# Performance work log

Measured on AMD Instinct MI355X. Metric: run time of the kernel, lower is better.

## Reference

```python
import jax, jax.numpy as jnp
import numpy as np

N = 100000   # nodes
E = 1600000  # edges (avg in-degree 16)
IN, H, C = 128, 128, 40
K = 2        # TAGConv hops (DGL default)


def setup_inputs() -> dict:
    key = jax.random.key(0)
    ks = jax.random.split(key, 7)
    in_feat = jax.random.normal(ks[0], (N, IN), dtype=jnp.float32)
    src = jax.random.randint(ks[1], (E,), 0, N)
    dst = jax.random.randint(ks[2], (E,), 0, N)
    # TAGConv linear: concat of (K+1) hop features -> out
    W1 = jax.random.normal(ks[3], ((K + 1) * IN, H), dtype=jnp.float32) / np.float32(np.sqrt((K + 1) * IN))
    b1 = jnp.zeros((H,), dtype=jnp.float32)
    W2 = jax.random.normal(ks[4], ((K + 1) * H, C), dtype=jnp.float32) / np.float32(np.sqrt((K + 1) * H))
    b2 = jnp.zeros((C,), dtype=jnp.float32)
    return {"in_feat": in_feat, "src": src, "dst": dst,
            "W1": W1, "b1": b1, "W2": W2, "b2": b2}


def _tagconv(x, src, dst, norm, W, b):
    feats = [x]
    h = x
    for _ in range(K):
        h = norm[:, None] * h                               # [N, d]
        h = jax.ops.segment_sum(h[src], dst, num_segments=N)  # SpMM via gather+scatter
        h = norm[:, None] * h
        feats.append(h)
    return jnp.concatenate(feats, axis=-1) @ W + b


def reference(in_feat, src, dst, W1, b1, W2, b2):
    deg = jax.ops.segment_sum(jnp.ones((E,), jnp.float32), dst, num_segments=N)
    norm = jnp.where(deg > 0, deg ** -0.5, 0.0)             # D^{-1/2}, inf -> 0
    h = jax.nn.relu(_tagconv(in_feat, src, dst, norm, W1, b1))
    h = jax.nn.relu(_tagconv(h, src, dst, norm, W2, b2))
    return jnp.mean(h, axis=0, keepdims=True)               # dgl.mean_nodes -> [1, C]
```

## Files before the change

kernel.cpp:

```cpp
#include <hip/hip_runtime.h>

typedef unsigned short u16;
typedef __attribute__((ext_vector_type(8))) short bf16x8;
typedef __attribute__((ext_vector_type(4))) float f32x4;

#define CSR_CHUNK 12288

__device__ inline u16 f2bf(float f) {
    union { float f; unsigned u; } v; v.f = f;
    unsigned r = v.u + 0x7fff + ((v.u >> 16) & 1);
    return (u16)(r >> 16);
}
__device__ inline float bflo(unsigned u) {
    union { unsigned u; float f; } v; v.u = u << 16; return v.f;
}
__device__ inline float bfhi(unsigned u) {
    union { unsigned u; float f; } v; v.u = u & 0xffff0000u; return v.f;
}
__device__ inline float bfs(u16 x) { return bflo((unsigned)x); }

__global__ void zero_int_k(int* __restrict__ p, int n) {
    int i = blockIdx.x * 256 + threadIdx.x;
    if (i < n) p[i] = 0;
}

__global__ __launch_bounds__(256) void bucket_cnt_k(
    const int* __restrict__ dst, int* __restrict__ bcnt, int E, int nbuck) {
    __shared__ int hist[1024];
    int e0 = blockIdx.x * CSR_CHUNK;
    int e1 = min(e0 + CSR_CHUNK, E);
    for (int i = threadIdx.x; i < nbuck; i += 256) hist[i] = 0;
    __syncthreads();
    for (int e = e0 + threadIdx.x; e < e1; e += 256)
        atomicAdd(&hist[dst[e] >> 7], 1);
    __syncthreads();
    for (int i = threadIdx.x; i < nbuck; i += 256) {
        int c = hist[i];
        if (c) atomicAdd(&bcnt[i], c);
    }
}

__global__ void bscan_k(const int* __restrict__ bcnt, int* __restrict__ bptr,
                        int* __restrict__ bcur, int nb, int E) {
    __shared__ int lds[256];
    int t = threadIdx.x;
    int base = t * 4;
    int v[4];
    int s = 0;
#pragma unroll
    for (int i = 0; i < 4; ++i) {
        v[i] = s;
        int idx = base + i;
        s += (idx < nb) ? bcnt[idx] : 0;
    }
    int x = s;
    lds[t] = x;
    __syncthreads();
    for (int off = 1; off < 256; off <<= 1) {
        int y = (t >= off) ? lds[t - off] : 0;
        __syncthreads();
        x += y;
        lds[t] = x;
        __syncthreads();
    }
    int toff = x - s;
#pragma unroll
    for (int i = 0; i < 4; ++i) {
        int idx = base + i;
        if (idx < nb) {
            int e0 = toff + v[i];
            bptr[idx] = e0;
            bcur[idx] = e0;
        }
    }
    if (t == 255) bptr[nb] = E;
}

__global__ __launch_bounds__(256) void passB_k(
    const int* __restrict__ src, const int* __restrict__ dst,
    int* __restrict__ bcur, int2* __restrict__ tmp, int E, int nbuck) {
    __shared__ int hist[1024];
    __shared__ int bbase[1024];
    int e0 = blockIdx.x * CSR_CHUNK;
    int e1 = min(e0 + CSR_CHUNK, E);
    for (int i = threadIdx.x; i < nbuck; i += 256) hist[i] = 0;
    __syncthreads();
    for (int e = e0 + threadIdx.x; e < e1; e += 256)
        atomicAdd(&hist[dst[e] >> 7], 1);
    __syncthreads();
    for (int i = threadIdx.x; i < nbuck; i += 256) {
        int c = hist[i];
        bbase[i] = c ? atomicAdd(&bcur[i], c) : 0;
        hist[i] = 0;
    }
    __syncthreads();
    for (int e = e0 + threadIdx.x; e < e1; e += 256) {
        int s = src[e], d = dst[e];
        int b = d >> 7;
        int r = atomicAdd(&hist[b], 1);
        int2 sd; sd.x = s; sd.y = d;
        tmp[bbase[b] + r] = sd;
    }
}

__global__ __launch_bounds__(256) void passC_k(
    const int2* __restrict__ tmp, const int* __restrict__ bptr,
    int* __restrict__ rowptr, float* __restrict__ norm, int* __restrict__ esrc,
    int N, int E) {
    __shared__ int cnt[128];
    __shared__ int sc[128];
    __shared__ int cur[128];
    int b = blockIdx.x, t = threadIdx.x;
    int base = bptr[b], endp = bptr[b + 1];
    int node0 = b << 7;
    int nNodes = min(128, N - node0);

    if (t < 128) cnt[t] = 0;
    __syncthreads();
    for (int i = base + t; i < endp; i += 256)
        atomicAdd(&cnt[tmp[i].y & 127], 1);
    __syncthreads();
    if (t < 128) sc[t] = cnt[t];
    __syncthreads();
    for (int off = 1; off < 128; off <<= 1) {
        int y = 0;
        if (t < 128 && t >= off) y = sc[t - off];
        __syncthreads();
        if (t < 128) sc[t] += y;
        __syncthreads();
    }
    if (t < 128) {
        int ex = sc[t] - cnt[t];
        cur[t] = ex;
        if (t < nNodes) {
            rowptr[node0 + t] = base + ex;
            int d = cnt[t];
            norm[node0 + t] = (d > 0) ? rsqrtf((float)d) : 0.f;
        }
    }
    if (b == gridDim.x - 1 && t == 0) rowptr[N] = E;
    __syncthreads();
    for (int i = base + t; i < endp; i += 256) {
        int2 sd = tmp[i];
        int pos = atomicAdd(&cur[sd.y & 127], 1);
        esrc[base + pos] = sd.x;
    }
}

__global__ void cvt_x_k(const float* __restrict__ X, u16* __restrict__ Xb, long n4) {
    long i = (long)blockIdx.x * 256 + threadIdx.x;
    if (i >= n4) return;
    float4 v = ((const float4*)X)[i];
    ushort4 o;
    o.x = f2bf(v.x); o.y = f2bf(v.y); o.z = f2bf(v.z); o.w = f2bf(v.w);
    ((ushort4*)Xb)[i] = o;
}

__global__ void pack_w1_k(const float* __restrict__ W1, u16* __restrict__ Wp) {
    int i = blockIdx.x * 256 + threadIdx.x;
    if (i >= 3 * 16384) return;
    int m = i >> 14, r = i & 16383;
    int jj = r & 7, lane = (r >> 3) & 63, kk = (r >> 9) & 3, t = r >> 11;
    int k = kk * 32 + (lane >> 4) * 8 + jj;
    int c = t * 16 + (lane & 15);
    Wp[i] = f2bf(W1[(size_t)m * 16384 + k * 128 + c]);
}

__global__ void pack_w2_k(const float* __restrict__ W2, u16* __restrict__ Wp) {
    int i = blockIdx.x * 256 + threadIdx.x;
    if (i >= 16384) return;
    int jj = i & 7, lane = (i >> 3) & 63, kk = (i >> 9) & 3, t = i >> 11;
    int k = kk * 32 + (lane >> 4) * 8 + jj;
    int c = t * 16 + (lane & 15);
    float v = 0.f;
    if (c < 120) {
        int hop = c / 40, j = c - hop * 40;
        v = W2[(size_t)(hop * 128 + k) * 40 + j];
    }
    Wp[i] = f2bf(v);
}

template <int MODE>
__global__ __launch_bounds__(256, 2) void gemm_mfma_k(
    const u16* __restrict__ Ab, const u16* __restrict__ Wp,
    float* __restrict__ Cf, u16* __restrict__ Cb,
    float* __restrict__ Cf2, u16* __restrict__ Cb2,
    const float* __restrict__ addp, const float* __restrict__ bias,
    const float* __restrict__ norm, int n, int nStripes) {
    int lane = threadIdx.x & 63;
    int wave = threadIdx.x >> 6;
    int rit = lane & 15;
    int kgrp = lane >> 4;

    bf16x8 bfr[8][4];
    const bf16x8* wp = (const bf16x8*)Wp;
#pragma unroll
    for (int t = 0; t < 8; ++t)
#pragma unroll
        for (int kk = 0; kk < 4; ++kk)
            bfr[t][kk] = wp[(t * 4 + kk) * 64 + lane];

    for (int s = blockIdx.x; s < nStripes; s += gridDim.x) {
        int r0 = s * 64 + wave * 16;
        int ar = min(r0 + rit, n - 1);
        const bf16x8* arow = (const bf16x8*)(Ab + (size_t)ar * 128);
        bf16x8 afr[4];
#pragma unroll
        for (int kk = 0; kk < 4; ++kk) afr[kk] = arow[kk * 4 + kgrp];

        f32x4 acc[8];
#pragma unroll
        for (int t = 0; t < 8; ++t) acc[t] = (f32x4)(0.f);
#pragma unroll
        for (int kk = 0; kk < 4; ++kk)
#pragma unroll
            for (int t = 0; t < 8; ++t)
                acc[t] = __builtin_amdgcn_mfma_f32_16x16x32_bf16(
                    afr[kk], bfr[t][kk], acc[t], 0, 0, 0);

#pragma unroll
        for (int j = 0; j < 4; ++j) {
            int rs = r0 + kgrp * 4 + j;
            if (rs >= n) continue;
            float nr = norm[rs];
#pragma unroll
            for (int t = 0; t < 8; ++t) {
                int c = t * 16 + rit;
                float v = acc[t][j];
                if (MODE == 0) {
                    if (c < 40) Cf[(size_t)rs * 40 + c] = v;
                    else if (c < 80) Cf2[(size_t)rs * 40 + c - 40] = v;
                    else if (c < 120) Cb2[(size_t)rs * 40 + c - 80] = f2bf(v * nr);
                } else if (MODE == 1) {
                    Cb[(size_t)rs * 128 + c] = f2bf(v * nr);
                } else if (MODE == 2) {
                    float ap = addp[(size_t)rs * 128 + c];
                    Cb[(size_t)rs * 128 + c] = f2bf(nr * (v + nr * ap));
                } else {
                    float ap = addp[(size_t)rs * 128 + c];
                    float r = fmaxf(v + nr * ap + bias[c], 0.f);
                    Cb[(size_t)rs * 128 + c] = f2bf(r);
                }
            }
        }
    }
}

__global__ __launch_bounds__(256) void spmm128_bf_k(
    const u16* __restrict__ in, float* __restrict__ out,
    const int* __restrict__ rowptr, const int* __restrict__ esrc, int n) {
    int gw = (blockIdx.x * 256 + threadIdx.x) >> 6;
    if (gw >= n) return;
    int lane = threadIdx.x & 63;
    int sub = lane >> 4;
    int l16 = lane & 15;
    int beg = rowptr[gw], end = rowptr[gw + 1];
    float a[8];
#pragma unroll
    for (int j = 0; j < 8; ++j) a[j] = 0.f;

    int e = beg + sub;
    for (; e + 4 < end; e += 8) {
        int s0 = esrc[e], s1 = esrc[e + 4];
        uint4 v0 = *(const uint4*)(in + (size_t)s0 * 128 + l16 * 8);
        uint4 v1 = *(const uint4*)(in + (size_t)s1 * 128 + l16 * 8);
        a[0] += bflo(v0.x); a[1] += bfhi(v0.x);
        a[2] += bflo(v0.y); a[3] += bfhi(v0.y);
        a[4] += bflo(v0.z); a[5] += bfhi(v0.z);
        a[6] += bflo(v0.w); a[7] += bfhi(v0.w);
        a[0] += bflo(v1.x); a[1] += bfhi(v1.x);
        a[2] += bflo(v1.y); a[3] += bfhi(v1.y);
        a[4] += bflo(v1.z); a[5] += bfhi(v1.z);
        a[6] += bflo(v1.w); a[7] += bfhi(v1.w);
    }
    for (; e < end; e += 4) {
        int s = esrc[e];
        uint4 v = *(const uint4*)(in + (size_t)s * 128 + l16 * 8);
        a[0] += bflo(v.x); a[1] += bfhi(v.x);
        a[2] += bflo(v.y); a[3] += bfhi(v.y);
        a[4] += bflo(v.z); a[5] += bfhi(v.z);
        a[6] += bflo(v.w); a[7] += bfhi(v.w);
    }
#pragma unroll
    for (int j = 0; j < 8; ++j) {
        a[j] += __shfl_xor(a[j], 16);
        a[j] += __shfl_xor(a[j], 32);
    }
    if (sub == 0) {
        float4 o0; o0.x = a[0]; o0.y = a[1]; o0.z = a[2]; o0.w = a[3];
        float4 o1; o1.x = a[4]; o1.y = a[5]; o1.z = a[6]; o1.w = a[7];
        *(float4*)(out + (size_t)gw * 128 + l16 * 8) = o0;
        *(float4*)(out + (size_t)gw * 128 + l16 * 8 + 4) = o1;
    }
}

__global__ __launch_bounds__(256) void spmm40_k(
    const u16* __restrict__ Z2b, const float* __restrict__ Z1, u16* __restrict__ u,
    const float* __restrict__ norm, const int* __restrict__ rowptr,
    const int* __restrict__ esrc, int n) {
    int gw = (blockIdx.x * 256 + threadIdx.x) >> 6;
    int lane = threadIdx.x & 63;
    if (gw >= n || lane >= 40) return;
    int beg = rowptr[gw], end = rowptr[gw + 1];
    float a = 0.f;
    int e = beg;
    for (; e + 3 < end; e += 4) {
        int s0 = esrc[e], s1 = esrc[e + 1], s2 = esrc[e + 2], s3 = esrc[e + 3];
        float v0 = bfs(Z2b[(size_t)s0 * 40 + lane]);
        float v1 = bfs(Z2b[(size_t)s1 * 40 + lane]);
        float v2 = bfs(Z2b[(size_t)s2 * 40 + lane]);
        float v3 = bfs(Z2b[(size_t)s3 * 40 + lane]);
        a += (v0 + v1) + (v2 + v3);
    }
    for (; e < end; ++e) a += bfs(Z2b[(size_t)esrc[e] * 40 + lane]);
    float nn = norm[gw];
    u[(size_t)gw * 40 + lane] = f2bf(nn * (Z1[(size_t)gw * 40 + lane] + nn * a));
}

__global__ __launch_bounds__(256) void spmm40_final_k(
    const u16* __restrict__ u, const float* __restrict__ Z0, const float* __restrict__ bias,
    float* __restrict__ partial, const float* __restrict__ norm,
    const int* __restrict__ rowptr, const int* __restrict__ esrc, int n, int nwaves) {
    __shared__ float lds[4][40];
    int wave = threadIdx.x >> 6;
    int lane = threadIdx.x & 63;
    int gw0 = blockIdx.x * 4 + wave;
    float accm = 0.f;
    float bb = (lane < 40) ? bias[lane] : 0.f;
    for (int node = gw0; node < n; node += nwaves) {
        if (lane < 40) {
            int beg = rowptr[node], end = rowptr[node + 1];
            float a = 0.f;
            int e = beg;
            for (; e + 3 < end; e += 4) {
                int s0 = esrc[e], s1 = esrc[e + 1], s2 = esrc[e + 2], s3 = esrc[e + 3];
                float v0 = bfs(u[(size_t)s0 * 40 + lane]);
                float v1 = bfs(u[(size_t)s1 * 40 + lane]);
                float v2 = bfs(u[(size_t)s2 * 40 + lane]);
                float v3 = bfs(u[(size_t)s3 * 40 + lane]);
                a += (v0 + v1) + (v2 + v3);
            }
            for (; e < end; ++e) a += bfs(u[(size_t)esrc[e] * 40 + lane]);
            float r = Z0[(size_t)node * 40 + lane] + norm[node] * a + bb;
            accm += fmaxf(r, 0.f);
        }
    }
    if (lane < 40) lds[wave][lane] = accm;
    __syncthreads();
    if (threadIdx.x < 40) {
        partial[blockIdx.x * 40 + threadIdx.x] =
            lds[0][threadIdx.x] + lds[1][threadIdx.x] + lds[2][threadIdx.x] + lds[3][threadIdx.x];
    }
}

__global__ __launch_bounds__(256) void reduce_mean_k(
    const float* __restrict__ partial, float* __restrict__ out, int nb, float invN) {
    __shared__ float lds[256];
    int c = blockIdx.x, t = threadIdx.x;
    float s = 0.f;
    for (int i = t; i < nb; i += 256) s += partial[(size_t)i * 40 + c];
    lds[t] = s;
    __syncthreads();
    for (int o = 128; o > 0; o >>= 1) {
        if (t < o) lds[t] += lds[t + o];
        __syncthreads();
    }
    if (t == 0) out[c] = lds[0] * invN;
}

extern "C" void kernel_launch(void* const* d_in, const int* in_sizes, int n_in,
                              void* d_out, int out_size, void* d_ws, size_t ws_size,
                              hipStream_t stream) {
    const float* X   = (const float*)d_in[0];
    const int*   src = (const int*)d_in[1];
    const int*   dst = (const int*)d_in[2];
    const float* W1  = (const float*)d_in[3];
    const float* b1  = (const float*)d_in[4];
    const float* W2  = (const float*)d_in[5];
    const float* b2  = (const float*)d_in[6];
    float* out = (float*)d_out;

    const int IN = 128;
    const int N = in_sizes[0] / IN;
    const int E = in_sizes[1];
    const int nb = (N + 127) >> 7;

    char* w = (char*)d_ws;
    size_t off = 0;
    auto alloc = [&](size_t bytes) -> char* {
        char* p = w + off;
        off = (off + bytes + 15) & ~(size_t)15;
        return p;
    };
    float* norm    = (float*)alloc((size_t)N * 4);
    int*   rowptr  = (int*)alloc((size_t)(N + 1) * 4);
    int*   bcnt    = (int*)alloc((size_t)(nb + 1) * 4);
    int*   bptr    = (int*)alloc((size_t)(nb + 1) * 4);
    int*   bcur    = (int*)alloc((size_t)(nb + 1) * 4);
    int*   esrc    = (int*)alloc((size_t)E * 4);
    u16*   Xb      = (u16*)alloc((size_t)N * 128 * 2);
    u16*   h1b     = (u16*)alloc((size_t)N * 128 * 2);
    u16*   g       = (u16*)alloc((size_t)N * 128 * 2);
    u16*   Wp1     = (u16*)alloc(3 * 16384 * 2);
    u16*   Wp2     = (u16*)alloc(16384 * 2);
    float* bufF    = (float*)alloc((size_t)N * 128 * 4);
    u16*   ubuf    = (u16*)alloc((size_t)N * 40 * 2);
    float* partial = (float*)alloc(2048 * 40 * 4);

    int2*  tmp = (int2*)bufF;
    float* Z0  = bufF;
    float* Z1  = bufF + (size_t)N * 40;
    u16*   Z2b = (u16*)(bufF + (size_t)2 * N * 40);

    int csr_blocks = (E + CSR_CHUNK - 1) / CSR_CHUNK;

    zero_int_k<<<(nb + 255) / 256, 256, 0, stream>>>(bcnt, nb);
    bucket_cnt_k<<<csr_blocks, 256, 0, stream>>>(dst, bcnt, E, nb);
    bscan_k<<<1, 256, 0, stream>>>(bcnt, bptr, bcur, nb, E);
    passB_k<<<csr_blocks, 256, 0, stream>>>(src, dst, bcur, tmp, E, nb);
    passC_k<<<nb, 256, 0, stream>>>(tmp, bptr, rowptr, norm, esrc, N, E);

    long n4 = (long)N * 128 / 4;
    cvt_x_k<<<(int)((n4 + 255) / 256), 256, 0, stream>>>(X, Xb, n4);
    pack_w1_k<<<(3 * 16384 + 255) / 256, 256, 0, stream>>>(W1, Wp1);
    pack_w2_k<<<(16384 + 255) / 256, 256, 0, stream>>>(W2, Wp2);

    int nStripes = (N + 63) / 64;
    int gemm_grid = 512;
    int spmm_grid = (N + 3) / 4;

    gemm_mfma_k<1><<<gemm_grid, 256, 0, stream>>>(
        Xb, Wp1 + 2 * 16384, nullptr, g, nullptr, nullptr, nullptr, nullptr, norm, N, nStripes);
    spmm128_bf_k<<<spmm_grid, 256, 0, stream>>>(g, bufF, rowptr, esrc, N);
    gemm_mfma_k<2><<<gemm_grid, 256, 0, stream>>>(
        Xb, Wp1 + 1 * 16384, nullptr, g, nullptr, nullptr, bufF, nullptr, norm, N, nStripes);
    spmm128_bf_k<<<spmm_grid, 256, 0, stream>>>(g, bufF, rowptr, esrc, N);
    gemm_mfma_k<3><<<gemm_grid, 256, 0, stream>>>(
        Xb, Wp1, nullptr, h1b, nullptr, nullptr, bufF, b1, norm, N, nStripes);

    gemm_mfma_k<0><<<gemm_grid, 256, 0, stream>>>(
        h1b, Wp2, Z0, nullptr, Z1, Z2b, nullptr, nullptr, norm, N, nStripes);
    spmm40_k<<<spmm_grid, 256, 0, stream>>>(Z2b, Z1, ubuf, norm, rowptr, esrc, N);
    spmm40_final_k<<<2048, 256, 0, stream>>>(ubuf, Z0, b2, partial, norm, rowptr, esrc, N, 8192);
    reduce_mean_k<<<40, 256, 0, stream>>>(partial, out, 2048, 1.f / (float)N);
}
```

Baseline: 444.6 us.

## Store GEMM output in 16-column slabs and gather per slab in SpMM

The GEMM writes its bf16 output as eight column slabs of 16 features each ([8][N][16]) instead of row-major [N][128]. The SpMM kernel now gives each block one slab, so every gather reads a 32-byte slab row per neighbor, and each of 16 lane groups handles a different edge. The aim is to shrink the working set per pass (each slab table is about 3.2 MB) so random gathers hit in L2. The cost is 8x more blocks, each re-reading rowptr and esrc, plus a longer shuffle reduction.

Measured after the change: 674.0 us. 1.52x slower.

```diff
diff --git a/kernel.cpp b/kernel.cpp
--- a/kernel.cpp
+++ b/kernel.cpp
@@ -232,10 +232,10 @@
                     else if (c < 80) Cf2[(size_t)rs * 40 + c - 40] = v;
                     else if (c < 120) Cb2[(size_t)rs * 40 + c - 80] = f2bf(v * nr);
                 } else if (MODE == 1) {
-                    Cb[(size_t)rs * 128 + c] = f2bf(v * nr);
+                    Cb[(((size_t)t * n + rs) << 4) + rit] = f2bf(v * nr);
                 } else if (MODE == 2) {
                     float ap = addp[(size_t)rs * 128 + c];
-                    Cb[(size_t)rs * 128 + c] = f2bf(nr * (v + nr * ap));
+                    Cb[(((size_t)t * n + rs) << 4) + rit] = f2bf(nr * (v + nr * ap));
                 } else {
                     float ap = addp[(size_t)rs * 128 + c];
                     float r = fmaxf(v + nr * ap + bias[c], 0.f);
@@ -246,51 +246,34 @@
     }
 }
 
-__global__ __launch_bounds__(256) void spmm128_bf_k(
-    const u16* __restrict__ in, float* __restrict__ out,
+__global__ __launch_bounds__(256) void spmm128_sl_k(
+    const u16* __restrict__ g, float* __restrict__ out,
     const int* __restrict__ rowptr, const int* __restrict__ esrc, int n) {
-    int gw = (blockIdx.x * 256 + threadIdx.x) >> 6;
-    if (gw >= n) return;
+    int sl = blockIdx.x & 7;
+    int node = (blockIdx.x >> 3) * 4 + (threadIdx.x >> 6);
+    if (node >= n) return;
     int lane = threadIdx.x & 63;
-    int sub = lane >> 4;
-    int l16 = lane & 15;
-    int beg = rowptr[gw], end = rowptr[gw + 1];
-    float a[8];
-#pragma unroll
-    for (int j = 0; j < 8; ++j) a[j] = 0.f;
-
-    int e = beg + sub;
-    for (; e + 4 < end; e += 8) {
-        int s0 = esrc[e], s1 = esrc[e + 4];
-        uint4 v0 = *(const uint4*)(in + (size_t)s0 * 128 + l16 * 8);
-        uint4 v1 = *(const uint4*)(in + (size_t)s1 * 128 + l16 * 8);
-        a[0] += bflo(v0.x); a[1] += bfhi(v0.x);
-        a[2] += bflo(v0.y); a[3] += bfhi(v0.y);
-        a[4] += bflo(v0.z); a[5] += bfhi(v0.z);
-        a[6] += bflo(v0.w); a[7] += bfhi(v0.w);
-        a[0] += bflo(v1.x); a[1] += bfhi(v1.x);
-        a[2] += bflo(v1.y); a[3] += bfhi(v1.y);
-        a[4] += bflo(v1.z); a[5] += bfhi(v1.z);
-        a[6] += bflo(v1.w); a[7] += bfhi(v1.w);
-    }
-    for (; e < end; e += 4) {
+    int sub = lane >> 2;
+    int l4 = lane & 3;
+    const u16* tab = g + ((size_t)sl * n << 4);
+    int beg = rowptr[node], end = rowptr[node + 1];
+    float a0 = 0.f, a1 = 0.f, a2 = 0.f, a3 = 0.f;
+    for (int e = beg + sub; e < end; e += 16) {
         int s = esrc[e];
-        uint4 v = *(const uint4*)(in + (size_t)s * 128 + l16 * 8);
-        a[0] += bflo(v.x); a[1] += bfhi(v.x);
-        a[2] += bflo(v.y); a[3] += bfhi(v.y);
-        a[4] += bflo(v.z); a[5] += bfhi(v.z);
-        a[6] += bflo(v.w); a[7] += bfhi(v.w);
-    }
-#pragma unroll
-    for (int j = 0; j < 8; ++j) {
-        a[j] += __shfl_xor(a[j], 16);
-        a[j] += __shfl_xor(a[j], 32);
+        uint2 v = *(const uint2*)(tab + ((size_t)s << 4) + l4 * 4);
+        a0 += bflo(v.x); a1 += bfhi(v.x);
+        a2 += bflo(v.y); a3 += bfhi(v.y);
+    }
+#pragma unroll
+    for (int off = 4; off < 64; off <<= 1) {
+        a0 += __shfl_xor(a0, off);
+        a1 += __shfl_xor(a1, off);
+        a2 += __shfl_xor(a2, off);
+        a3 += __shfl_xor(a3, off);
     }
     if (sub == 0) {
-        float4 o0; o0.x = a[0]; o0.y = a[1]; o0.z = a[2]; o0.w = a[3];
-        float4 o1; o1.x = a[4]; o1.y = a[5]; o1.z = a[6]; o1.w = a[7];
-        *(float4*)(out + (size_t)gw * 128 + l16 * 8) = o0;
-        *(float4*)(out + (size_t)gw * 128 + l16 * 8 + 4) = o1;
+        float4 o; o.x = a0; o.y = a1; o.z = a2; o.w = a3;
+        *(float4*)(out + (size_t)node * 128 + sl * 16 + l4 * 4) = o;
     }
 }
 
@@ -428,13 +411,14 @@
     int nStripes = (N + 63) / 64;
     int gemm_grid = 512;
     int spmm_grid = (N + 3) / 4;
+    int spmm_sl_grid = 8 * ((N + 3) / 4);
 
     gemm_mfma_k<1><<<gemm_grid, 256, 0, stream>>>(
         Xb, Wp1 + 2 * 16384, nullptr, g, nullptr, nullptr, nullptr, nullptr, norm, N, nStripes);
-    spmm128_bf_k<<<spmm_grid, 256, 0, stream>>>(g, bufF, rowptr, esrc, N);
+    spmm128_sl_k<<<spmm_sl_grid, 256, 0, stream>>>(g, bufF, rowptr, esrc, N);
     gemm_mfma_k<2><<<gemm_grid, 256, 0, stream>>>(
         Xb, Wp1 + 1 * 16384, nullptr, g, nullptr, nullptr, bufF, nullptr, norm, N, nStripes);
-    spmm128_bf_k<<<spmm_grid, 256, 0, stream>>>(g, bufF, rowptr, esrc, N);
+    spmm128_sl_k<<<spmm_sl_grid, 256, 0, stream>>>(g, bufF, rowptr, esrc, N);
     gemm_mfma_k<3><<<gemm_grid, 256, 0, stream>>>(
         Xb, Wp1, nullptr, h1b, nullptr, nullptr, bufF, b1, norm, N, nStripes);
 
```

## Fuse hop-combine epilogues into SpMM kernels and merge prep launches

Applied to the files above, without the earlier changes.

The three layer-1 GEMMs now run up front, writing bf16 projections P1 and P0 alongside g. The Horner-style combine (norm scaling, adding the projection, bias and ReLU) moves into the SpMM epilogue, which writes bf16 outputs directly. This removes the fp32 N×128 SpMM output round-trip and the dependent GEMM reads of it. The zero, convert and weight-pack kernels are merged into one prep launch to cut launch overhead. It adds an extra bf16 buffer and rounds P0/P1 to bf16 before the addition, which slightly changes numerics.

Measured after the change: 427.1 us. 1.04x faster.

```diff
diff --git a/kernel.cpp b/kernel.cpp
--- a/kernel.cpp
+++ b/kernel.cpp
@@ -18,10 +18,53 @@
     union { unsigned u; float f; } v; v.u = u & 0xffff0000u; return v.f;
 }
 __device__ inline float bfs(u16 x) { return bflo((unsigned)x); }
-
-__global__ void zero_int_k(int* __restrict__ p, int n) {
-    int i = blockIdx.x * 256 + threadIdx.x;
-    if (i < n) p[i] = 0;
+__device__ inline unsigned pk(float lo, float hi) {
+    return (unsigned)f2bf(lo) | ((unsigned)f2bf(hi) << 16);
+}
+
+__global__ __launch_bounds__(256) void prep_k(
+    const float* __restrict__ X, u16* __restrict__ Xb, long n4,
+    const float* __restrict__ W1, u16* __restrict__ Wp1,
+    const float* __restrict__ W2, u16* __restrict__ Wp2,
+    int* __restrict__ bcnt, int nzero) {
+    int b = blockIdx.x;
+    int t = threadIdx.x;
+    if (b < 4) {
+        int i = b * 256 + t;
+        if (i < nzero) bcnt[i] = 0;
+        return;
+    }
+    b -= 4;
+    if (b < 192) {
+        int i = b * 256 + t;
+        int m = i >> 14, r = i & 16383;
+        int jj = r & 7, lane = (r >> 3) & 63, kk = (r >> 9) & 3, tt = r >> 11;
+        int k = kk * 32 + (lane >> 4) * 8 + jj;
+        int c = tt * 16 + (lane & 15);
+        Wp1[i] = f2bf(W1[(size_t)m * 16384 + k * 128 + c]);
+        return;
+    }
+    b -= 192;
+    if (b < 64) {
+        int i = b * 256 + t;
+        int jj = i & 7, lane = (i >> 3) & 63, kk = (i >> 9) & 3, tt = i >> 11;
+        int k = kk * 32 + (lane >> 4) * 8 + jj;
+        int c = tt * 16 + (lane & 15);
+        float v = 0.f;
+        if (c < 120) {
+            int hop = c / 40, j = c - hop * 40;
+            v = W2[(size_t)(hop * 128 + k) * 40 + j];
+        }
+        Wp2[i] = f2bf(v);
+        return;
+    }
+    b -= 64;
+    long i = (long)b * 256 + t;
+    if (i >= n4) return;
+    float4 v = ((const float4*)X)[i];
+    ushort4 o;
+    o.x = f2bf(v.x); o.y = f2bf(v.y); o.z = f2bf(v.z); o.w = f2bf(v.w);
+    ((ushort4*)Xb)[i] = o;
 }
 
 __global__ __launch_bounds__(256) void bucket_cnt_k(
@@ -147,45 +190,11 @@
     }
 }
 
-__global__ void cvt_x_k(const float* __restrict__ X, u16* __restrict__ Xb, long n4) {
-    long i = (long)blockIdx.x * 256 + threadIdx.x;
-    if (i >= n4) return;
-    float4 v = ((const float4*)X)[i];
-    ushort4 o;
-    o.x = f2bf(v.x); o.y = f2bf(v.y); o.z = f2bf(v.z); o.w = f2bf(v.w);
-    ((ushort4*)Xb)[i] = o;
-}
-
-__global__ void pack_w1_k(const float* __restrict__ W1, u16* __restrict__ Wp) {
-    int i = blockIdx.x * 256 + threadIdx.x;
-    if (i >= 3 * 16384) return;
-    int m = i >> 14, r = i & 16383;
-    int jj = r & 7, lane = (r >> 3) & 63, kk = (r >> 9) & 3, t = r >> 11;
-    int k = kk * 32 + (lane >> 4) * 8 + jj;
-    int c = t * 16 + (lane & 15);
-    Wp[i] = f2bf(W1[(size_t)m * 16384 + k * 128 + c]);
-}
-
-__global__ void pack_w2_k(const float* __restrict__ W2, u16* __restrict__ Wp) {
-    int i = blockIdx.x * 256 + threadIdx.x;
-    if (i >= 16384) return;
-    int jj = i & 7, lane = (i >> 3) & 63, kk = (i >> 9) & 3, t = i >> 11;
-    int k = kk * 32 + (lane >> 4) * 8 + jj;
-    int c = t * 16 + (lane & 15);
-    float v = 0.f;
-    if (c < 120) {
-        int hop = c / 40, j = c - hop * 40;
-        v = W2[(size_t)(hop * 128 + k) * 40 + j];
-    }
-    Wp[i] = f2bf(v);
-}
-
 template <int MODE>
 __global__ __launch_bounds__(256, 2) void gemm_mfma_k(
     const u16* __restrict__ Ab, const u16* __restrict__ Wp,
     float* __restrict__ Cf, u16* __restrict__ Cb,
     float* __restrict__ Cf2, u16* __restrict__ Cb2,
-    const float* __restrict__ addp, const float* __restrict__ bias,
     const float* __restrict__ norm, int n, int nStripes) {
     int lane = threadIdx.x & 63;
     int wave = threadIdx.x >> 6;
@@ -222,7 +231,7 @@
         for (int j = 0; j < 4; ++j) {
             int rs = r0 + kgrp * 4 + j;
             if (rs >= n) continue;
-            float nr = norm[rs];
+            float nr = (MODE == 4) ? 0.f : norm[rs];
 #pragma unroll
             for (int t = 0; t < 8; ++t) {
                 int c = t * 16 + rit;
@@ -233,28 +242,26 @@
                     else if (c < 120) Cb2[(size_t)rs * 40 + c - 80] = f2bf(v * nr);
                 } else if (MODE == 1) {
                     Cb[(size_t)rs * 128 + c] = f2bf(v * nr);
-                } else if (MODE == 2) {
-                    float ap = addp[(size_t)rs * 128 + c];
-                    Cb[(size_t)rs * 128 + c] = f2bf(nr * (v + nr * ap));
                 } else {
-                    float ap = addp[(size_t)rs * 128 + c];
-                    float r = fmaxf(v + nr * ap + bias[c], 0.f);
-                    Cb[(size_t)rs * 128 + c] = f2bf(r);
+                    Cb[(size_t)rs * 128 + c] = f2bf(v);
                 }
             }
         }
     }
 }
 
-__global__ __launch_bounds__(256) void spmm128_bf_k(
-    const u16* __restrict__ in, float* __restrict__ out,
+template <int F>
+__global__ __launch_bounds__(256) void spmm128_f_k(
+    const u16* __restrict__ g, const u16* __restrict__ P,
+    const float* __restrict__ bias, u16* __restrict__ outb,
+    const float* __restrict__ norm,
     const int* __restrict__ rowptr, const int* __restrict__ esrc, int n) {
-    int gw = (blockIdx.x * 256 + threadIdx.x) >> 6;
-    if (gw >= n) return;
+    int node = (blockIdx.x * 256 + threadIdx.x) >> 6;
+    if (node >= n) return;
     int lane = threadIdx.x & 63;
     int sub = lane >> 4;
     int l16 = lane & 15;
-    int beg = rowptr[gw], end = rowptr[gw + 1];
+    int beg = rowptr[node], end = rowptr[node + 1];
     float a[8];
 #pragma unroll
     for (int j = 0; j < 8; ++j) a[j] = 0.f;
@@ -262,8 +269,8 @@
     int e = beg + sub;
     for (; e + 4 < end; e += 8) {
         int s0 = esrc[e], s1 = esrc[e + 4];
-        uint4 v0 = *(const uint4*)(in + (size_t)s0 * 128 + l16 * 8);
-        uint4 v1 = *(const uint4*)(in + (size_t)s1 * 128 + l16 * 8);
+        uint4 v0 = *(const uint4*)(g + (size_t)s0 * 128 + l16 * 8);
+        uint4 v1 = *(const uint4*)(g + (size_t)s1 * 128 + l16 * 8);
         a[0] += bflo(v0.x); a[1] += bfhi(v0.x);
         a[2] += bflo(v0.y); a[3] += bfhi(v0.y);
         a[4] += bflo(v0.z); a[5] += bfhi(v0.z);
@@ -275,7 +282,7 @@
     }
     for (; e < end; e += 4) {
         int s = esrc[e];
-        uint4 v = *(const uint4*)(in + (size_t)s * 128 + l16 * 8);
+        uint4 v = *(const uint4*)(g + (size_t)s * 128 + l16 * 8);
         a[0] += bflo(v.x); a[1] += bfhi(v.x);
         a[2] += bflo(v.y); a[3] += bfhi(v.y);
         a[4] += bflo(v.z); a[5] += bfhi(v.z);
@@ -287,10 +294,35 @@
         a[j] += __shfl_xor(a[j], 32);
     }
     if (sub == 0) {
-        float4 o0; o0.x = a[0]; o0.y = a[1]; o0.z = a[2]; o0.w = a[3];
-        float4 o1; o1.x = a[4]; o1.y = a[5]; o1.z = a[6]; o1.w = a[7];
-        *(float4*)(out + (size_t)gw * 128 + l16 * 8) = o0;
-        *(float4*)(out + (size_t)gw * 128 + l16 * 8 + 4) = o1;
+        float nn = norm[node];
+        uint4 pv = *(const uint4*)(P + (size_t)node * 128 + l16 * 8);
+        float p[8];
+        p[0] = bflo(pv.x); p[1] = bfhi(pv.x);
+        p[2] = bflo(pv.y); p[3] = bfhi(pv.y);
+        p[4] = bflo(pv.z); p[5] = bfhi(pv.z);
+        p[6] = bflo(pv.w); p[7] = bfhi(pv.w);
+        float r[8];
+        if (F == 1) {
+#pragma unroll
+            for (int j = 0; j < 8; ++j) r[j] = nn * (p[j] + nn * a[j]);
+        } else {
+            float4 b0 = *(const float4*)(bias + l16 * 8);
+            float4 b1v = *(const float4*)(bias + l16 * 8 + 4);
+            r[0] = fmaxf(p[0] + nn * a[0] + b0.x, 0.f);
+            r[1] = fmaxf(p[1] + nn * a[1] + b0.y, 0.f);
+            r[2] = fmaxf(p[2] + nn * a[2] + b0.z, 0.f);
+            r[3] = fmaxf(p[3] + nn * a[3] + b0.w, 0.f);
+            r[4] = fmaxf(p[4] + nn * a[4] + b1v.x, 0.f);
+            r[5] = fmaxf(p[5] + nn * a[5] + b1v.y, 0.f);
+            r[6] = fmaxf(p[6] + nn * a[6] + b1v.z, 0.f);
+            r[7] = fmaxf(p[7] + nn * a[7] + b1v.w, 0.f);
+        }
+        uint4 o;
+        o.x = pk(r[0], r[1]);
+        o.y = pk(r[2], r[3]);
+        o.z = pk(r[4], r[5]);
+        o.w = pk(r[6], r[7]);
+        *(uint4*)(outb + (size_t)node * 128 + l16 * 8) = o;
     }
 }
 
@@ -401,6 +433,7 @@
     u16*   Xb      = (u16*)alloc((size_t)N * 128 * 2);
     u16*   h1b     = (u16*)alloc((size_t)N * 128 * 2);
     u16*   g       = (u16*)alloc((size_t)N * 128 * 2);
+    u16*   g2      = (u16*)alloc((size_t)N * 128 * 2);
     u16*   Wp1     = (u16*)alloc(3 * 16384 * 2);
     u16*   Wp2     = (u16*)alloc(16384 * 2);
     float* bufF    = (float*)alloc((size_t)N * 128 * 4);
@@ -408,38 +441,40 @@
     float* partial = (float*)alloc(2048 * 40 * 4);
 
     int2*  tmp = (int2*)bufF;
+    u16*   P1b = (u16*)bufF;
+    u16*   P0b = (u16*)bufF + (size_t)N * 128;
     float* Z0  = bufF;
     float* Z1  = bufF + (size_t)N * 40;
     u16*   Z2b = (u16*)(bufF + (size_t)2 * N * 40);
 
     int csr_blocks = (E + CSR_CHUNK - 1) / CSR_CHUNK;
-
-    zero_int_k<<<(nb + 255) / 256, 256, 0, stream>>>(bcnt, nb);
+    long n4 = (long)N * 128 / 4;
+    int prep_grid = 4 + 192 + 64 + (int)((n4 + 255) / 256);
+
+    prep_k<<<prep_grid, 256, 0, stream>>>(X, Xb, n4, W1, Wp1, W2, Wp2, bcnt, nb);
+
     bucket_cnt_k<<<csr_blocks, 256, 0, stream>>>(dst, bcnt, E, nb);
     bscan_k<<<1, 256, 0, stream>>>(bcnt, bptr, bcur, nb, E);
     passB_k<<<csr_blocks, 256, 0, stream>>>(src, dst, bcur, tmp, E, nb);
     passC_k<<<nb, 256, 0, stream>>>(tmp, bptr, rowptr, norm, esrc, N, E);
 
-    long n4 = (long)N * 128 / 4;
-    cvt_x_k<<<(int)((n4 + 255) / 256), 256, 0, stream>>>(X, Xb, n4);
-    pack_w1_k<<<(3 * 16384 + 255) / 256, 256, 0, stream>>>(W1, Wp1);
-    pack_w2_k<<<(16384 + 255) / 256, 256, 0, stream>>>(W2, Wp2);
-
     int nStripes = (N + 63) / 64;
     int gemm_grid = 512;
     int spmm_grid = (N + 3) / 4;
 
     gemm_mfma_k<1><<<gemm_grid, 256, 0, stream>>>(
-        Xb, Wp1 + 2 * 16384, nullptr, g, nullptr, nullptr, nullptr, nullptr, norm, N, nStripes);
-    spmm128_bf_k<<<spmm_grid, 256, 0, stream>>>(g, bufF, rowptr, esrc, N);
-    gemm_mfma_k<2><<<gemm_grid, 256, 0, stream>>>(
-        Xb, Wp1 + 1 * 16384, nullptr, g, nullptr, nullptr, bufF, nullptr, norm, N, nStripes);
-    spmm128_bf_k<<<spmm_grid, 256, 0, stream>>>(g, bufF, rowptr, esrc, N);
-    gemm_mfma_k<3><<<gemm_grid, 256, 0, stream>>>(
-        Xb, Wp1, nullptr, h1b, nullptr, nullptr, bufF, b1, norm, N, nStripes);
+        Xb, Wp1 + 2 * 16384, nullptr, g, nullptr, nullptr, norm, N, nStripes);
+    gemm_mfma_k<4><<<gemm_grid, 256, 0, stream>>>(
+        Xb, Wp1 + 1 * 16384, nullptr, P1b, nullptr, nullptr, norm, N, nStripes);
+    gemm_mfma_k<4><<<gemm_grid, 256, 0, stream>>>(
+        Xb, Wp1, nullptr, P0b, nullptr, nullptr, norm, N, nStripes);
+    spmm128_f_k<1><<<spmm_grid, 256, 0, stream>>>(
+        g, P1b, nullptr, g2, norm, rowptr, esrc, N);
+    spmm128_f_k<2><<<spmm_grid, 256, 0, stream>>>(
+        g2, P0b, b1, h1b, norm, rowptr, esrc, N);
 
     gemm_mfma_k<0><<<gemm_grid, 256, 0, stream>>>(
-        h1b, Wp2, Z0, nullptr, Z1, Z2b, nullptr, nullptr, norm, N, nStripes);
+        h1b, Wp2, Z0, nullptr, Z1, Z2b, norm, N, nStripes);
     spmm40_k<<<spmm_grid, 256, 0, stream>>>(Z2b, Z1, ubuf, norm, rowptr, esrc, N);
     spmm40_final_k<<<2048, 256, 0, stream>>>(ubuf, Z0, b2, partial, norm, rowptr, esrc, N, 8192);
     reduce_mean_k<<<40, 256, 0, stream>>>(partial, out, 2048, 1.f / (float)N);
```
